# Kernel tuning notes

Hardware: AMD Instinct MI355X
Metric: run time of the kernel (lower is better)

## Reference

```python
import jax, jax.numpy as jnp
import numpy as np

N = 100000       # nodes
E = 1000000      # edges
IN = 128         # in_dim
HID = 64         # hid_dim
NET = 4          # n_etypes
STEPS = 5        # n_steps
G = 128          # graphs in batch
LBL = 10         # num_labels


def setup_inputs() -> dict:
    key = jax.random.key(0)
    ks = jax.random.split(key, 20)
    def w(k, shape, fan_in):
        return jax.random.normal(k, shape, jnp.float32) / np.sqrt(fan_in)
    return dict(
        x=jax.random.normal(ks[0], (N, IN), jnp.float32),
        src=jax.random.randint(ks[1], (E,), 0, N),
        dst=jax.random.randint(ks[2], (E,), 0, N),
        etype=jax.random.randint(ks[3], (E,), 0, NET),
        node2graph=jnp.sort(jax.random.randint(ks[4], (N,), 0, G)),
        # linear_in
        W_in=w(ks[5], (HID, IN), IN), b_in=jnp.zeros((HID,), jnp.float32),
        # per-edge-type linears [n_etypes, out, in]
        We=w(ks[6], (NET, HID, HID), HID), be=jnp.zeros((NET, HID), jnp.float32),
        # GRUCell (torch layout: rows = [r; z; n])
        W_ih=w(ks[7], (3 * HID, HID), HID), b_ih=jnp.zeros((3 * HID,), jnp.float32),
        W_hh=w(ks[8], (3 * HID, HID), HID), b_hh=jnp.zeros((3 * HID,), jnp.float32),
        # classifier
        W1=w(ks[9], (HID // 2, HID), HID), b1=jnp.zeros((HID // 2,), jnp.float32),
        W2=w(ks[10], (LBL, HID // 2), HID // 2), b2=jnp.zeros((LBL,), jnp.float32),
    )


def reference(x, W_in, b_in, We, be, W_ih, b_ih, W_hh, b_hh, W1, b1, W2, b2,
              src, dst, etype, node2graph):
    h = x @ W_in.T + b_in                                  # [N, HID]
    for _ in range(STEPS):
        # per-etype linear on node states: trans[e] = h @ We[e].T + be[e]
        trans = jnp.einsum('nd,efd->enf', h, We) + be[:, None, :]  # [NET, N, HID]
        msgs = trans[etype, src]                           # [E, HID] gather per edge
        a = jax.ops.segment_sum(msgs, dst, num_segments=N)  # scatter-add aggregation
        # GRUCell(a, h)
        gi = a @ W_ih.T + b_ih
        gh = h @ W_hh.T + b_hh
        ir, iz, i_n = jnp.split(gi, 3, axis=-1)
        hr, hz, h_n = jnp.split(gh, 3, axis=-1)
        r = jax.nn.sigmoid(ir + hr)
        z = jax.nn.sigmoid(iz + hz)
        n = jnp.tanh(i_n + r * h_n)
        h = (1.0 - z) * n + z * h
    # dgl.mean_nodes: per-graph mean of node states
    cnt = jnp.maximum(jax.ops.segment_sum(jnp.ones((N,), h.dtype), node2graph, num_segments=G), 1.0)
    hg = jax.ops.segment_sum(h, node2graph, num_segments=G) / cnt[:, None]  # [G, HID]
    return jax.nn.relu(hg @ W1.T + b1) @ W2.T + b2         # [G, LBL]
```

## Files before the change

### kernel.cpp

```cpp
#include <hip/hip_runtime.h>
#include <hip/hip_bf16.h>
#include <math.h>

#define N_NODES 100000
#define N_EDGES 1000000
#define IN_DIM 128
#define HID 64
#define NET 4
#define STEPS 5
#define G_GRAPHS 128
#define LBL 10
#define NGRP 6250
#define NGRP_PAD 6256

typedef __attribute__((ext_vector_type(8))) short short8;
typedef __attribute__((ext_vector_type(4))) float f32x4;
typedef unsigned short ushort_t;

__device__ inline ushort_t f2bf(float v) {
    __hip_bfloat16 b = __float2bfloat16(v);
    return __builtin_bit_cast(ushort_t, b);
}
__device__ inline float bf2f(ushort_t u) {
    __hip_bfloat16 b = __builtin_bit_cast(__hip_bfloat16, u);
    return __bfloat162float(b);
}


__global__ void k_pack_b1(const float* __restrict__ We, const float* __restrict__ be,
                          ushort_t* __restrict__ B1, float* __restrict__ bs1) {
    int idx = blockIdx.x * blockDim.x + threadIdx.x;
    if (idx >= 6 * 16 * 4 * 16 * 8) return;
    int j = idx & 7, u = (idx >> 3) & 15, g = (idx >> 7) & 3, ct = (idx >> 9) & 15, s = idx >> 13;
    int m = ct * 16 + u;
    int t = m >> 6, o = m & 63;
    int sk = (s < 2) ? s : (s < 4) ? (s - 2) : (s - 4);
    int k = sk * 32 + g * 8 + j;
    float val = We[t * 4096 + o * 64 + k];
    ushort_t hi = f2bf(val);
    B1[idx] = (s < 4) ? hi : f2bf(val - bf2f(hi));
    if (s == 0 && g == 0 && j == 0) bs1[m] = be[t * 64 + o];
}

__global__ void k_pack_b2(const float* __restrict__ W_ih, const float* __restrict__ b_ih,
                          const float* __restrict__ W_hh, const float* __restrict__ b_hh,
                          ushort_t* __restrict__ B2, float* __restrict__ bg2) {
    int idx = blockIdx.x * blockDim.x + threadIdx.x;
    if (idx >= 12 * 16 * 4 * 16 * 8) return;
    int j = idx & 7, u = (idx >> 3) & 15, g = (idx >> 7) & 3, ct = (idx >> 9) & 15, s = idx >> 13;
    int m = ct * 16 + u;
    int q = m >> 6, gate = (m >> 4) & 3, c = q * 16 + (m & 15);
    int k = (s & 3) * 32 + g * 8 + j;
    float val;
    if (gate == 0)      { int jr = c;        val = (k < 64) ? W_ih[jr * 64 + k] : W_hh[jr * 64 + k - 64]; }
    else if (gate == 1) { int jr = 64 + c;   val = (k < 64) ? W_ih[jr * 64 + k] : W_hh[jr * 64 + k - 64]; }
    else if (gate == 2) { int jr = 128 + c;  val = (k < 64) ? W_ih[jr * 64 + k] : 0.f; }
    else                { int jr = 128 + c;  val = (k < 64) ? 0.f : W_hh[jr * 64 + k - 64]; }
    ushort_t hi = f2bf(val);
    B2[idx] = (s < 8) ? hi : f2bf(val - bf2f(hi));
    if (s == 0 && g == 0 && j == 0) {
        float bv;
        if (gate == 0)      bv = b_ih[c] + b_hh[c];
        else if (gate == 1) bv = b_ih[64 + c] + b_hh[64 + c];
        else if (gate == 2) bv = b_ih[128 + c];
        else                bv = b_hh[128 + c];
        bg2[m] = bv;
    }
}

__global__ void k_pack_bin(const float* __restrict__ W_in, ushort_t* __restrict__ BIN) {
    int idx = blockIdx.x * blockDim.x + threadIdx.x;
    if (idx >= 24576) return;
    int j = idx & 7, lu = (idx >> 3) & 63, ct = (idx >> 9) & 3, s = idx >> 11;
    int g = lu >> 4, u = lu & 15;
    int m = ct * 16 + u;
    int k = (s & 3) * 32 + g * 8 + j;
    float val = W_in[m * 128 + k];
    ushort_t hi = f2bf(val);
    BIN[idx] = (s < 8) ? hi : f2bf(val - bf2f(hi));
}

__global__ __launch_bounds__(256) void k_linear_in(const float* __restrict__ x,
        const ushort_t* __restrict__ BIN, const float* __restrict__ b_in,
        ushort_t* __restrict__ AH) {
    __shared__ float hlds[4][16 * 68];
    int tid = threadIdx.x;
    int lane = tid & 63, wp = tid >> 6;
    int g = lane >> 4, u = lane & 15;
    int grp = blockIdx.x * 4 + wp;
    bool ok = grp < NGRP;
    int row = ok ? (grp * 16 + u) : 0;
    short8 xhi[4], xlo[4];
    #pragma unroll
    for (int ks = 0; ks < 4; ++ks) {
        const float* xp = &x[(size_t)row * 128 + ks * 32 + g * 8];
        float4 v0 = ok ? *(const float4*)xp : make_float4(0.f, 0.f, 0.f, 0.f);
        float4 v1 = ok ? *(const float4*)(xp + 4) : make_float4(0.f, 0.f, 0.f, 0.f);
        float vv[8] = {v0.x, v0.y, v0.z, v0.w, v1.x, v1.y, v1.z, v1.w};
        #pragma unroll
        for (int j = 0; j < 8; ++j) {
            ushort_t hh = f2bf(vv[j]);
            xhi[ks][j] = (short)hh;
            xlo[ks][j] = (short)f2bf(vv[j] - bf2f(hh));
        }
    }
    f32x4 zero = {0.f, 0.f, 0.f, 0.f};
    f32x4 acc[4] = {zero, zero, zero, zero};
    #pragma unroll
    for (int s = 0; s < 12; ++s) {
        int ks = s & 3;
        short8 af = (s < 4) ? xhi[ks] : (s < 8) ? xlo[ks] : xhi[ks];
        #pragma unroll
        for (int ct = 0; ct < 4; ++ct) {
            short8 bf = *(const short8*)&BIN[((size_t)(s * 4 + ct) * 64 + lane) * 8];
            acc[ct] = __builtin_amdgcn_mfma_f32_16x16x32_bf16(af, bf, acc[ct], 0, 0, 0);
        }
    }
    #pragma unroll
    for (int ct = 0; ct < 4; ++ct) {
        float bo = b_in[ct * 16 + u];
        #pragma unroll
        for (int j = 0; j < 4; ++j)
            hlds[wp][(g * 4 + j) * 68 + ct * 16 + u] = acc[ct][j] + bo;
    }
    __syncthreads();
    #pragma unroll
    for (int k = 0; k < 4; ++k) {
        int bi = g + 4 * k;
        short8 ov;
        #pragma unroll
        for (int j = 0; j < 8; ++j) {
            float v = hlds[wp][u * 68 + (bi & 7) * 8 + j];
            ushort_t hh = f2bf(v);
            ov[j] = (bi < 8) ? (short)hh : (short)f2bf(v - bf2f(hh));
        }
        int blk = (bi < 8) ? (8 + bi) : (24 + (bi - 8));
        if (ok) *(short8*)&AH[((size_t)grp * 32 + blk) * 128 + u * 8] = ov;
    }
}

__global__ void k_hist(const int* __restrict__ dst, int* __restrict__ deg) {
    int e = blockIdx.x * blockDim.x + threadIdx.x;
    if (e < N_EDGES) atomicAdd(&deg[dst[e]], 1);
}

__global__ __launch_bounds__(256) void k_scan1(const int* __restrict__ deg,
        int* __restrict__ ex, int* __restrict__ bsum, int n) {
    __shared__ int ts[256];
    int base = blockIdx.x * 1024;
    int vals[4]; int s = 0;
    #pragma unroll
    for (int i = 0; i < 4; ++i) {
        int idx = base + threadIdx.x * 4 + i;
        vals[i] = (idx < n) ? deg[idx] : 0;
        s += vals[i];
    }
    ts[threadIdx.x] = s;
    __syncthreads();
    for (int off = 1; off < 256; off <<= 1) {
        int v = (threadIdx.x >= off) ? ts[threadIdx.x - off] : 0;
        __syncthreads();
        ts[threadIdx.x] += v;
        __syncthreads();
    }
    int run = (threadIdx.x == 0) ? 0 : ts[threadIdx.x - 1];
    #pragma unroll
    for (int i = 0; i < 4; ++i) {
        int idx = base + threadIdx.x * 4 + i;
        if (idx < n) ex[idx] = run;
        run += vals[i];
    }
    if (threadIdx.x == 255) bsum[blockIdx.x] = ts[255];
}

__global__ void k_scan2(int* bsum, int nb, int* row_ptr_end) {
    if (threadIdx.x == 0 && blockIdx.x == 0) {
        int run = 0;
        for (int i = 0; i < nb; ++i) { int t = bsum[i]; bsum[i] = run; run += t; }
        *row_ptr_end = run;
    }
}

__global__ void k_scan3(int* __restrict__ row_ptr, int* __restrict__ cursor,
                        const int* __restrict__ bsum, int n) {
    int i = blockIdx.x * blockDim.x + threadIdx.x;
    if (i < n) {
        int v = row_ptr[i] + bsum[i >> 10];
        row_ptr[i] = v;
        cursor[i] = v;
    }
}

__global__ void k_fill(const int* __restrict__ src, const int* __restrict__ dst,
                       const int* __restrict__ et, int* __restrict__ cursor,
                       int* __restrict__ adj) {
    int e = blockIdx.x * blockDim.x + threadIdx.x;
    if (e < N_EDGES) {
        int d = dst[e];
        int p = atomicAdd(&cursor[d], 1);
        adj[p] = src[e] | (et[e] << 20);
    }
}

__global__ __launch_bounds__(512) void k_mm1(const ushort_t* __restrict__ AH,
        const ushort_t* __restrict__ B1, const float* __restrict__ bs1,
        ushort_t* __restrict__ trans) {
    __shared__ ushort_t lds[16896];
    int tid = threadIdx.x;
    size_t gb = (size_t)blockIdx.x * 8;
    #pragma unroll
    for (int it = 0; it < 4; ++it) {
        int f = it * 512 + tid;
        int gl = f >> 8, part = (f >> 7) & 1, inner = f & 127;
        size_t srcp = ((gb + gl) * 32 + (part ? 24 : 8)) * 128 + (size_t)inner * 8;
        *(short8*)&lds[f * 8] = *(const short8*)&AH[srcp];
    }
    __syncthreads();
    int lane = tid & 63, wp = tid >> 6;
    int q = wp & 3, rp = wp >> 2;
    int g = lane >> 4, u = lane & 15;
    int n0 = blockIdx.x * 128;
    f32x4 zero = {0.f, 0.f, 0.f, 0.f};
    f32x4 acc[4][4];
    #pragma unroll
    for (int i = 0; i < 4; ++i)
        #pragma unroll
        for (int j = 0; j < 4; ++j) acc[i][j] = zero;
    #pragma unroll
    for (int s = 0; s < 6; ++s) {
        int part = (s == 2 || s == 3) ? 1 : 0;
        int lb = ((s & 1) ? 4 : 0) + g;
        short8 bfr[4], afr[4];
        #pragma unroll
        for (int ct = 0; ct < 4; ++ct)
            bfr[ct] = *(const short8*)&B1[((size_t)(s * 16 + q * 4 + ct) * 64 + g * 16 + u) * 8];
        #pragma unroll
        for (int rt = 0; rt < 4; ++rt) {
            int gl = rp * 4 + rt;
            afr[rt] = *(const short8*)&lds[((gl * 2 + part) * 8 + lb) * 128 + u * 8];
        }
        #pragma unroll
        for (int rt = 0; rt < 4; ++rt)
            #pragma unroll
            for (int ct = 0; ct < 4; ++ct)
                acc[rt][ct] = __builtin_amdgcn_mfma_f32_16x16x32_bf16(afr[rt], bfr[ct], acc[rt][ct], 0, 0, 0);
    }
    float bsv[4];
    #pragma unroll
    for (int ct = 0; ct < 4; ++ct) bsv[ct] = bs1[q * 64 + ct * 16 + u];
    #pragma unroll
    for (int h = 0; h < 2; ++h) {
        __syncthreads();
        if (rp == h) {
            #pragma unroll
            for (int rt = 0; rt < 4; ++rt)
                #pragma unroll
                for (int ct = 0; ct < 4; ++ct)
                    #pragma unroll
                    for (int j = 0; j < 4; ++j) {
                        int rl = rt * 16 + g * 4 + j;
                        lds[rl * 264 + q * 64 + ct * 16 + u] = f2bf(acc[rt][ct][j] + bsv[ct]);
                    }
        }
        __syncthreads();
        int rl = tid >> 3, seg = tid & 7;
        int n = n0 + h * 64 + rl;
        if (n < N_NODES) {
            #pragma unroll
            for (int i = 0; i < 4; ++i) {
                short8 v = *(const short8*)&lds[rl * 264 + seg * 32 + i * 8];
                *(short8*)&trans[(size_t)n * 256 + seg * 32 + i * 8] = v;
            }
        }
    }
}

__global__ __launch_bounds__(512) void k_mm2(ushort_t* __restrict__ AH,
        const ushort_t* __restrict__ B2, const float* __restrict__ bg2) {
    __shared__ ushort_t lds[32768];
    int tid = threadIdx.x;
    size_t base = (size_t)blockIdx.x * 8 * 4096;
    #pragma unroll
    for (int it = 0; it < 8; ++it) {
        int f = it * 512 + tid;
        *(short8*)&lds[f * 8] = *(const short8*)&AH[base + (size_t)f * 8];
    }
    __syncthreads();
    int lane = tid & 63, wp = tid >> 6;
    int q = wp & 3, rp = wp >> 2;
    int g = lane >> 4, u = lane & 15;
    f32x4 zero = {0.f, 0.f, 0.f, 0.f};
    f32x4 acc[4][4];
    #pragma unroll
    for (int i = 0; i < 4; ++i)
        #pragma unroll
        for (int j = 0; j < 4; ++j) acc[i][j] = zero;
    const int bb2[12] = {0, 4, 8, 12, 16, 20, 24, 28, 0, 4, 8, 12};
    #pragma unroll
    for (int s = 0; s < 12; ++s) {
        short8 bfr[4], afr[4];
        #pragma unroll
        for (int ct = 0; ct < 4; ++ct)
            bfr[ct] = *(const short8*)&B2[((size_t)(s * 16 + q * 4 + ct) * 64 + g * 16 + u) * 8];
        #pragma unroll
        for (int rt = 0; rt < 4; ++rt) {
            int gl = rp * 4 + rt;
            afr[rt] = *(const short8*)&lds[(gl * 32 + bb2[s] + g) * 128 + u * 8];
        }
        #pragma unroll
        for (int rt = 0; rt < 4; ++rt)
            #pragma unroll
            for (int ct = 0; ct < 4; ++ct)
                acc[rt][ct] = __builtin_amdgcn_mfma_f32_16x16x32_bf16(afr[rt], bfr[ct], acc[rt][ct], 0, 0, 0);
    }
    __syncthreads();
    float bgv[4];
    #pragma unroll
    for (int ct = 0; ct < 4; ++ct) bgv[ct] = bg2[q * 64 + ct * 16 + u];
    int hid = q * 16 + u;
    int bhi = 8 + (hid >> 3), blo = 24 + (hid >> 3), el = hid & 7;
    #pragma unroll
    for (int rt = 0; rt < 4; ++rt) {
        int gl = rp * 4 + rt;
        #pragma unroll
        for (int j = 0; j < 4; ++j) {
            int uu = g * 4 + j;
            int shi = (gl * 32 + bhi) * 128 + uu * 8 + el;
            int slo = (gl * 32 + blo) * 128 + uu * 8 + el;
            float ho = bf2f(lds[shi]) + bf2f(lds[slo]);
            float rs  = acc[rt][0][j] + bgv[0];
            float zs  = acc[rt][1][j] + bgv[1];
            float inn = acc[rt][2][j] + bgv[2];
            float hnn = acc[rt][3][j] + bgv[3];
            float r = 1.f / (1.f + __expf(-rs));
            float z = 1.f / (1.f + __expf(-zs));
            float t = inn + r * hnn;
            float e2 = __expf(2.f * t);
            float nn = 1.f - 2.f / (e2 + 1.f);
            float hnew = (1.f - z) * nn + z * ho;
            ushort_t hh = f2bf(hnew);
            lds[shi] = hh;
            lds[slo] = f2bf(hnew - bf2f(hh));
        }
    }
    __syncthreads();
    #pragma unroll
    for (int it = 0; it < 4; ++it) {
        int c = it * 512 + tid;
        int gl = c >> 8, r = c & 255, bi = r >> 4, uu = r & 15;
        int blk = (bi < 8) ? (8 + bi) : (16 + bi);
        int lofs = (gl * 32 + blk) * 128 + uu * 8;
        short8 v = *(const short8*)&lds[lofs];
        *(short8*)&AH[base + (size_t)lofs] = v;
    }
}

__global__ __launch_bounds__(1024) void k_aggregate(const int* __restrict__ row_ptr,
        const int* __restrict__ adj, const ushort_t* __restrict__ trans,
        ushort_t* __restrict__ AH) {
    __shared__ float alds[16 * 72];
    int w = threadIdx.x >> 6, lane = threadIdx.x & 63;
    int grp = blockIdx.x;
    int n = grp * 16 + w;
    int beg = row_ptr[n], end = row_ptr[n + 1];
    float a0 = 0.f, a1 = 0.f, a2 = 0.f, a3 = 0.f;
    int i = beg;
    for (; i + 8 <= end; i += 8) {
        int pk[8];
        #pragma unroll
        for (int t = 0; t < 8; ++t) pk[t] = adj[i + t];
        float v[8];
        #pragma unroll
        for (int t = 0; t < 8; ++t)
            v[t] = bf2f(trans[(size_t)(pk[t] & 0xFFFFF) * 256 + (pk[t] >> 20) * 64 + lane]);
        a0 += v[0] + v[4]; a1 += v[1] + v[5]; a2 += v[2] + v[6]; a3 += v[3] + v[7];
    }
    for (; i + 2 <= end; i += 2) {
        int pk0 = adj[i], pk1 = adj[i + 1];
        a0 += bf2f(trans[(size_t)(pk0 & 0xFFFFF) * 256 + (pk0 >> 20) * 64 + lane]);
        a1 += bf2f(trans[(size_t)(pk1 & 0xFFFFF) * 256 + (pk1 >> 20) * 64 + lane]);
    }
    if (i < end) {
        int pk = adj[i];
        a2 += bf2f(trans[(size_t)(pk & 0xFFFFF) * 256 + (pk >> 20) * 64 + lane]);
    }
    alds[w * 72 + lane] = (a0 + a1) + (a2 + a3);
    __syncthreads();
    if (threadIdx.x < 256) {
        int bi = threadIdx.x >> 4, u = threadIdx.x & 15;
        int b8 = bi & 7;
        bool ishi = bi < 8;
        short8 ov;
        #pragma unroll
        for (int j = 0; j < 8; ++j) {
            float v = alds[u * 72 + b8 * 8 + j];
            ushort_t hh = f2bf(v);
            ov[j] = ishi ? (short)hh : (short)f2bf(v - bf2f(hh));
        }
        *(short8*)&AH[((size_t)grp * 32 + (ishi ? b8 : 16 + b8)) * 128 + u * 8] = ov;
    }
}

__global__ __launch_bounds__(256) void k_pool(const int* __restrict__ n2g,
        const ushort_t* __restrict__ AH, float* __restrict__ hg) {
    int gidx = blockIdx.x;
    int lo = 0, hi = N_NODES;
    while (lo < hi) { int mid = (lo + hi) >> 1; if (n2g[mid] < gidx) lo = mid + 1; else hi = mid; }
    int s = lo;
    hi = N_NODES;
    while (lo < hi) { int mid = (lo + hi) >> 1; if (n2g[mid] < gidx + 1) lo = mid + 1; else hi = mid; }
    int e = lo;
    int w = threadIdx.x >> 6, lane = threadIdx.x & 63;
    int bh = 8 + (lane >> 3), bl = 24 + (lane >> 3), el = lane & 7;
    float sum = 0.f;
    for (int n = s + w; n < e; n += 4) {
        size_t base = (size_t)(n >> 4) * 4096 + (size_t)(n & 15) * 8;
        sum += bf2f(AH[base + bh * 128 + el]) + bf2f(AH[base + bl * 128 + el]);
    }
    __shared__ float red[4][64];
    red[w][lane] = sum;
    __syncthreads();
    if (threadIdx.x < 64) {
        float tot = red[0][lane] + red[1][lane] + red[2][lane] + red[3][lane];
        float cnt = (float)(e - s);
        hg[gidx * 64 + lane] = tot / fmaxf(cnt, 1.f);
    }
}

__global__ __launch_bounds__(64) void k_cls(const float* __restrict__ hg,
        const float* __restrict__ W1, const float* __restrict__ b1,
        const float* __restrict__ W2, const float* __restrict__ b2,
        float* __restrict__ out) {
    int gidx = blockIdx.x;
    __shared__ float v[64];
    __shared__ float m[32];
    v[threadIdx.x] = hg[gidx * 64 + threadIdx.x];
    __syncthreads();
    if (threadIdx.x < 32) {
        float a = b1[threadIdx.x];
        #pragma unroll 8
        for (int k = 0; k < 64; ++k) a = fmaf(v[k], W1[threadIdx.x * 64 + k], a);
        m[threadIdx.x] = fmaxf(a, 0.f);
    }
    __syncthreads();
    if (threadIdx.x < 10) {
        float a = b2[threadIdx.x];
        #pragma unroll
        for (int j = 0; j < 32; ++j) a = fmaf(m[j], W2[threadIdx.x * 32 + j], a);
        out[gidx * 10 + threadIdx.x] = a;
    }
}

extern "C" void kernel_launch(void* const* d_in, const int* in_sizes, int n_in,
                              void* d_out, int out_size, void* d_ws, size_t ws_size,
                              hipStream_t stream) {
    const float* x    = (const float*)d_in[0];
    const int* src    = (const int*)d_in[1];
    const int* dst    = (const int*)d_in[2];
    const int* etype  = (const int*)d_in[3];
    const int* n2g    = (const int*)d_in[4];
    const float* W_in = (const float*)d_in[5];
    const float* b_in = (const float*)d_in[6];
    const float* We   = (const float*)d_in[7];
    const float* be   = (const float*)d_in[8];
    const float* W_ih = (const float*)d_in[9];
    const float* b_ih = (const float*)d_in[10];
    const float* W_hh = (const float*)d_in[11];
    const float* b_hh = (const float*)d_in[12];
    const float* W1   = (const float*)d_in[13];
    const float* b1   = (const float*)d_in[14];
    const float* W2   = (const float*)d_in[15];
    const float* b2   = (const float*)d_in[16];
    float* out = (float*)d_out;

    char* wsb = (char*)d_ws;
    size_t off = 0;
    auto alloc = [&](size_t bytes) -> void* {
        void* p = wsb + off;
        off += (bytes + 255) & ~(size_t)255;
        return p;
    };
    ushort_t* AH      = (ushort_t*)alloc((size_t)NGRP_PAD * 4096 * 2);
    ushort_t* trans   = (ushort_t*)alloc((size_t)N_NODES * 256 * 2);
    int*      adj     = (int*)     alloc((size_t)N_EDGES * 4);
    int*      row_ptr = (int*)     alloc((size_t)(N_NODES + 1) * 4);
    int*      cursor  = (int*)     alloc((size_t)N_NODES * 4);
    int*      deg     = (int*)     alloc((size_t)N_NODES * 4);
    int*      bsum    = (int*)     alloc(1024);
    ushort_t* B1      = (ushort_t*)alloc((size_t)6 * 16 * 4 * 16 * 8 * 2);
    float*    bs1     = (float*)   alloc(256 * 4);
    ushort_t* B2      = (ushort_t*)alloc((size_t)12 * 16 * 4 * 16 * 8 * 2);
    float*    bg2     = (float*)   alloc(256 * 4);
    ushort_t* BIN     = (ushort_t*)alloc((size_t)24576 * 2);
    float*    hg      = (float*)   alloc(128 * 64 * 4);

    hipMemsetAsync(AH + (size_t)NGRP * 4096, 0, (size_t)(NGRP_PAD - NGRP) * 4096 * 2, stream);

    hipLaunchKernelGGL(k_pack_b1, dim3(192), dim3(256), 0, stream, We, be, B1, bs1);
    hipLaunchKernelGGL(k_pack_b2, dim3(384), dim3(256), 0, stream, W_ih, b_ih, W_hh, b_hh, B2, bg2);
    hipLaunchKernelGGL(k_pack_bin, dim3(96), dim3(256), 0, stream, W_in, BIN);
    hipLaunchKernelGGL(k_linear_in, dim3((NGRP + 3) / 4), dim3(256), 0, stream, x, BIN, b_in, AH);

    hipMemsetAsync(deg, 0, (size_t)N_NODES * 4, stream);
    hipLaunchKernelGGL(k_hist, dim3((N_EDGES + 255) / 256), dim3(256), 0, stream, dst, deg);
    int nblk = (N_NODES + 1023) / 1024;
    hipLaunchKernelGGL(k_scan1, dim3(nblk), dim3(256), 0, stream, deg, row_ptr, bsum, N_NODES);
    hipLaunchKernelGGL(k_scan2, dim3(1), dim3(64), 0, stream, bsum, nblk, row_ptr + N_NODES);
    hipLaunchKernelGGL(k_scan3, dim3((N_NODES + 255) / 256), dim3(256), 0, stream, row_ptr, cursor, bsum, N_NODES);
    hipLaunchKernelGGL(k_fill, dim3((N_EDGES + 255) / 256), dim3(256), 0, stream, src, dst, etype, cursor, adj);

    int gblk = NGRP_PAD / 8;
    for (int step = 0; step < STEPS; ++step) {
        hipLaunchKernelGGL(k_mm1, dim3(gblk), dim3(512), 0, stream, AH, B1, bs1, trans);
        hipLaunchKernelGGL(k_aggregate, dim3(NGRP), dim3(1024), 0, stream, row_ptr, adj, trans, AH);
        hipLaunchKernelGGL(k_mm2, dim3(gblk), dim3(512), 0, stream, AH, B2, bg2);
    }
    hipLaunchKernelGGL(k_pool, dim3(G_GRAPHS), dim3(256), 0, stream, n2g, AH, hg);
    hipLaunchKernelGGL(k_cls, dim3(G_GRAPHS), dim3(64), 0, stream, hg, W1, b1, W2, b2, out);
}
```

Before: 964.0 us.

## Build CSR adjacency via two-level bucketed counting sort instead of global atomics

Replaces the per-node histogram, three-kernel scan and atomic fill with a bucketed radix-style build. Edges are first binned into 1024 buckets of 128 destination nodes, using shared-memory histograms and staged coalesced scatter. A per-bucket kernel then sorts each bucket by node in LDS to emit adj and row_ptr. This targets the scattered global atomics and random writes of the original CSR build, at the cost of an extra edge buffer pass and more complex kernels. Edge order within a node becomes different but sums are order-insensitive up to float rounding.

```diff
diff --git a/kernel.cpp b/kernel.cpp
--- a/kernel.cpp
+++ b/kernel.cpp
@@ -12,6 +12,8 @@
 #define LBL 10
 #define NGRP 6250
 #define NGRP_PAD 6256
+#define NBKT 1024
+#define TILE_E 8192
 
 typedef __attribute__((ext_vector_type(8))) short short8;
 typedef __attribute__((ext_vector_type(4))) float f32x4;
@@ -139,66 +141,130 @@
     }
 }
 
-__global__ void k_hist(const int* __restrict__ dst, int* __restrict__ deg) {
-    int e = blockIdx.x * blockDim.x + threadIdx.x;
-    if (e < N_EDGES) atomicAdd(&deg[dst[e]], 1);
-}
-
-__global__ __launch_bounds__(256) void k_scan1(const int* __restrict__ deg,
-        int* __restrict__ ex, int* __restrict__ bsum, int n) {
-    __shared__ int ts[256];
-    int base = blockIdx.x * 1024;
-    int vals[4]; int s = 0;
-    #pragma unroll
-    for (int i = 0; i < 4; ++i) {
-        int idx = base + threadIdx.x * 4 + i;
-        vals[i] = (idx < n) ? deg[idx] : 0;
-        s += vals[i];
-    }
-    ts[threadIdx.x] = s;
-    __syncthreads();
-    for (int off = 1; off < 256; off <<= 1) {
-        int v = (threadIdx.x >= off) ? ts[threadIdx.x - off] : 0;
-        __syncthreads();
-        ts[threadIdx.x] += v;
-        __syncthreads();
-    }
-    int run = (threadIdx.x == 0) ? 0 : ts[threadIdx.x - 1];
-    #pragma unroll
-    for (int i = 0; i < 4; ++i) {
-        int idx = base + threadIdx.x * 4 + i;
-        if (idx < n) ex[idx] = run;
-        run += vals[i];
-    }
-    if (threadIdx.x == 255) bsum[blockIdx.x] = ts[255];
-}
-
-__global__ void k_scan2(int* bsum, int nb, int* row_ptr_end) {
-    if (threadIdx.x == 0 && blockIdx.x == 0) {
-        int run = 0;
-        for (int i = 0; i < nb; ++i) { int t = bsum[i]; bsum[i] = run; run += t; }
-        *row_ptr_end = run;
-    }
-}
-
-__global__ void k_scan3(int* __restrict__ row_ptr, int* __restrict__ cursor,
-                        const int* __restrict__ bsum, int n) {
-    int i = blockIdx.x * blockDim.x + threadIdx.x;
-    if (i < n) {
-        int v = row_ptr[i] + bsum[i >> 10];
-        row_ptr[i] = v;
-        cursor[i] = v;
-    }
-}
-
-__global__ void k_fill(const int* __restrict__ src, const int* __restrict__ dst,
-                       const int* __restrict__ et, int* __restrict__ cursor,
-                       int* __restrict__ adj) {
-    int e = blockIdx.x * blockDim.x + threadIdx.x;
-    if (e < N_EDGES) {
-        int d = dst[e];
-        int p = atomicAdd(&cursor[d], 1);
-        adj[p] = src[e] | (et[e] << 20);
+
+__global__ __launch_bounds__(256) void k_bhist(const int* __restrict__ dst,
+        int* __restrict__ bhist) {
+    __shared__ int h[NBKT];
+    for (int i = threadIdx.x; i < NBKT; i += 256) h[i] = 0;
+    __syncthreads();
+    int idx = blockIdx.x * 256 + threadIdx.x;
+    for (int e = idx; e < N_EDGES; e += 256 * 256) atomicAdd(&h[dst[e] >> 7], 1);
+    __syncthreads();
+    for (int i = threadIdx.x; i < NBKT; i += 256) {
+        int c = h[i];
+        if (c) atomicAdd(&bhist[i], c);
+    }
+}
+
+__global__ __launch_bounds__(1024) void k_bscan(const int* __restrict__ bhist,
+        int* __restrict__ bbase, int* __restrict__ bcursor) {
+    __shared__ int ts[NBKT];
+    int t = threadIdx.x;
+    int v = bhist[t];
+    ts[t] = v;
+    __syncthreads();
+    for (int off = 1; off < NBKT; off <<= 1) {
+        int u = (t >= off) ? ts[t - off] : 0;
+        __syncthreads();
+        ts[t] += u;
+        __syncthreads();
+    }
+    int excl = ts[t] - v;
+    bbase[t] = excl;
+    bcursor[t] = excl;
+    if (t == NBKT - 1) bbase[NBKT] = ts[NBKT - 1];
+}
+
+__global__ __launch_bounds__(512) void k_bscatter(const int* __restrict__ src,
+        const int* __restrict__ dst, const int* __restrict__ et,
+        int* __restrict__ bcursor, unsigned int* __restrict__ ebuf) {
+    __shared__ int hcnt[NBKT], loff[NBKT], gpos[NBKT], ps[512];
+    __shared__ unsigned int stage[TILE_E];
+    __shared__ unsigned short sbkt[TILE_E];
+    int tid = threadIdx.x;
+    int base = blockIdx.x * TILE_E;
+    int tilecnt = min(TILE_E, N_EDGES - base);
+    for (int i = tid; i < NBKT; i += 512) hcnt[i] = 0;
+    __syncthreads();
+    #pragma unroll
+    for (int k = 0; k < TILE_E / 512; ++k) {
+        int e = base + tid + k * 512;
+        if (e < N_EDGES) atomicAdd(&hcnt[dst[e] >> 7], 1);
+    }
+    __syncthreads();
+    int c0 = hcnt[tid * 2], c1 = hcnt[tid * 2 + 1];
+    ps[tid] = c0 + c1;
+    __syncthreads();
+    for (int off = 1; off < 512; off <<= 1) {
+        int u = (tid >= off) ? ps[tid - off] : 0;
+        __syncthreads();
+        ps[tid] += u;
+        __syncthreads();
+    }
+    int ex = ps[tid] - (c0 + c1);
+    loff[tid * 2] = ex;
+    loff[tid * 2 + 1] = ex + c0;
+    for (int b = tid; b < NBKT; b += 512) {
+        int c = hcnt[b];
+        gpos[b] = c ? atomicAdd(&bcursor[b], c) : 0;
+    }
+    __syncthreads();
+    for (int i = tid; i < NBKT; i += 512) hcnt[i] = 0;
+    __syncthreads();
+    #pragma unroll
+    for (int k = 0; k < TILE_E / 512; ++k) {
+        int e = base + tid + k * 512;
+        if (e < N_EDGES) {
+            int d = dst[e];
+            int b = d >> 7;
+            int r = atomicAdd(&hcnt[b], 1);
+            int lp = loff[b] + r;
+            stage[lp] = (unsigned int)src[e] | ((unsigned int)et[e] << 20)
+                      | ((unsigned int)(d & 127) << 22);
+            sbkt[lp] = (unsigned short)b;
+        }
+    }
+    __syncthreads();
+    for (int i = tid; i < tilecnt; i += 512) {
+        int b = sbkt[i];
+        ebuf[gpos[b] + (i - loff[b])] = stage[i];
+    }
+}
+
+__global__ __launch_bounds__(256) void k_bcsr(const unsigned int* __restrict__ ebuf,
+        const int* __restrict__ bbase, int* __restrict__ adj, int* __restrict__ row_ptr) {
+    __shared__ int ncnt[128], noff[129], nps[128];
+    int b = blockIdx.x;
+    int tid = threadIdx.x;
+    int ebeg = bbase[b], eend = bbase[b + 1];
+    int ecnt = eend - ebeg;
+    if (tid < 128) ncnt[tid] = 0;
+    __syncthreads();
+    for (int i = tid; i < ecnt; i += 256) atomicAdd(&ncnt[(ebuf[ebeg + i] >> 22) & 127], 1);
+    __syncthreads();
+    int v = (tid < 128) ? ncnt[tid] : 0;
+    if (tid < 128) nps[tid] = v;
+    __syncthreads();
+    for (int off = 1; off < 128; off <<= 1) {
+        int u = (tid >= off && tid < 128) ? nps[tid - off] : 0;
+        __syncthreads();
+        if (tid < 128) nps[tid] += u;
+        __syncthreads();
+    }
+    if (tid < 128) noff[tid] = nps[tid] - v;
+    if (tid == 127) noff[128] = nps[127];
+    __syncthreads();
+    if (tid < 128) ncnt[tid] = 0;
+    __syncthreads();
+    for (int i = tid; i < ecnt; i += 256) {
+        unsigned int p = ebuf[ebeg + i];
+        int nl = (p >> 22) & 127;
+        int r = atomicAdd(&ncnt[nl], 1);
+        adj[ebeg + noff[nl] + r] = (int)(p & 0x3FFFFF);
+    }
+    for (int i = tid; i <= 128; i += 256) {
+        int n = b * 128 + i;
+        if (n <= N_NODES) row_ptr[n] = ebeg + noff[i];
     }
 }
 
@@ -483,10 +549,11 @@
     ushort_t* AH      = (ushort_t*)alloc((size_t)NGRP_PAD * 4096 * 2);
     ushort_t* trans   = (ushort_t*)alloc((size_t)N_NODES * 256 * 2);
     int*      adj     = (int*)     alloc((size_t)N_EDGES * 4);
+    unsigned int* ebuf = (unsigned int*)alloc((size_t)N_EDGES * 4);
     int*      row_ptr = (int*)     alloc((size_t)(N_NODES + 1) * 4);
-    int*      cursor  = (int*)     alloc((size_t)N_NODES * 4);
-    int*      deg     = (int*)     alloc((size_t)N_NODES * 4);
-    int*      bsum    = (int*)     alloc(1024);
+    int*      bhist   = (int*)     alloc((size_t)NBKT * 4);
+    int*      bbase   = (int*)     alloc((size_t)(NBKT + 1) * 4);
+    int*      bcursor = (int*)     alloc((size_t)NBKT * 4);
     ushort_t* B1      = (ushort_t*)alloc((size_t)6 * 16 * 4 * 16 * 8 * 2);
     float*    bs1     = (float*)   alloc(256 * 4);
     ushort_t* B2      = (ushort_t*)alloc((size_t)12 * 16 * 4 * 16 * 8 * 2);
@@ -501,13 +568,12 @@
     hipLaunchKernelGGL(k_pack_bin, dim3(96), dim3(256), 0, stream, W_in, BIN);
     hipLaunchKernelGGL(k_linear_in, dim3((NGRP + 3) / 4), dim3(256), 0, stream, x, BIN, b_in, AH);
 
-    hipMemsetAsync(deg, 0, (size_t)N_NODES * 4, stream);
-    hipLaunchKernelGGL(k_hist, dim3((N_EDGES + 255) / 256), dim3(256), 0, stream, dst, deg);
-    int nblk = (N_NODES + 1023) / 1024;
-    hipLaunchKernelGGL(k_scan1, dim3(nblk), dim3(256), 0, stream, deg, row_ptr, bsum, N_NODES);
-    hipLaunchKernelGGL(k_scan2, dim3(1), dim3(64), 0, stream, bsum, nblk, row_ptr + N_NODES);
-    hipLaunchKernelGGL(k_scan3, dim3((N_NODES + 255) / 256), dim3(256), 0, stream, row_ptr, cursor, bsum, N_NODES);
-    hipLaunchKernelGGL(k_fill, dim3((N_EDGES + 255) / 256), dim3(256), 0, stream, src, dst, etype, cursor, adj);
+    hipMemsetAsync(bhist, 0, (size_t)NBKT * 4, stream);
+    hipLaunchKernelGGL(k_bhist, dim3(256), dim3(256), 0, stream, dst, bhist);
+    hipLaunchKernelGGL(k_bscan, dim3(1), dim3(1024), 0, stream, bhist, bbase, bcursor);
+    hipLaunchKernelGGL(k_bscatter, dim3((N_EDGES + TILE_E - 1) / TILE_E), dim3(512), 0, stream,
+                       src, dst, etype, bcursor, ebuf);
+    hipLaunchKernelGGL(k_bcsr, dim3(NBKT), dim3(256), 0, stream, ebuf, bbase, adj, row_ptr);
 
     int gblk = NGRP_PAD / 8;
     for (int step = 0; step < STEPS; ++step) {
```

Result: faster. 877.0 us (-9.0%).
